# Performance work log

Hardware: AMD Instinct MI355X
Metric: run time of the kernel (lower is better)

## Reference

```python
import jax, jax.numpy as jnp
import numpy as np

jax.config.update("jax_enable_x64", True)  # original uses torch fp64 for the reciprocal trick

# --- GenericE layout constants ---
N = 32            # NUM_POSITIONS
D = 128           # per-position feature dim
F = N * D         # flattened dim
B = 8192          # batch
NIB_A, NIB_B = 0, 1
SLOT_DIVIDEND, SLOT_DIVISOR, SLOT_REMAINDER, SLOT_QUOTIENT = 2, 3, 4, 5
OP_START, OPCODE, BASE = 64, 3, 2
S = 60.0          # DIV_SCALE
SM_S = 60.0       # SOFTMAX1_SCALE
OP_FLAT = 0 * D + OP_START + OPCODE  # flat index of opcode channel at position 0


def _build_weights():
    # ClearDivSlotsFFN: hidden_dim = 4 slots * 2 units; bake_clear_pair wiring
    cW_up = np.zeros((8, F), np.float32)
    cW_gate = np.zeros((8, F), np.float32)
    cW_down = np.zeros((F, 8), np.float32)
    for i, slot in enumerate([SLOT_DIVIDEND, SLOT_DIVISOR, SLOT_REMAINDER, SLOT_QUOTIENT]):
        h = 2 * i
        # delta[slot] = -(1/S) * relu(S*op_w) * slot_val  -> clears slot when opcode active
        cW_up[h, OP_FLAT] = S
        cW_gate[h, slot] = 1.0
        cW_down[slot, h] = -1.0 / S
        # guard unit of the pair (zero down weight, mirrors gather's guard unit)
        cW_up[h + 1, OP_FLAT] = -S
        cW_gate[h + 1, slot] = -1.0
    # GatherScalarFFN: hidden_dim = N + 1; wiring straight from the source
    H = N + 1
    gW_up = np.zeros((H, F), np.float32)
    gW_gate = np.zeros((H, F), np.float32)
    gW_down = np.zeros((F, H), np.float32)
    dst = 0 * D + SLOT_DIVIDEND
    for i in range(N):
        gW_up[i, OP_FLAT] = S
        gW_gate[i, i * D + NIB_A] = float(BASE ** i)
        gW_down[dst, i] = 1.0 / S
    gW_up[N, OP_FLAT] = -S
    gW_gate[N, dst] = -1.0
    # gW_down[dst, N] = 0.0 (explicit in source)
    return (jnp.asarray(cW_up), jnp.asarray(cW_gate), jnp.asarray(cW_down),
            jnp.asarray(gW_up), jnp.asarray(gW_gate), jnp.asarray(gW_down))


def setup_inputs() -> dict:
    key = jax.random.key(0)
    x = jax.random.uniform(key, (B, N, D), dtype=jnp.float32)
    cW_up, cW_gate, cW_down, gW_up, gW_gate, gW_down = _build_weights()
    base_powers = jnp.asarray([float(BASE ** j) for j in range(N)], dtype=jnp.float64)
    return {"x": x, "cW_up": cW_up, "cW_gate": cW_gate, "cW_down": cW_down,
            "gW_up": gW_up, "gW_gate": gW_gate, "gW_down": gW_down,
            "base_powers": base_powers}


def _ffn_delta(xf, W_up, W_gate, W_down):
    # GenericFlattenedFFN residual delta: W_down @ (relu(W_up x) * (W_gate x))
    h = jax.nn.relu(xf @ W_up.T) * (xf @ W_gate.T)   # [B, H]
    return h @ W_down.T                               # [B, F]


def reference(x, cW_up, cW_gate, cW_down, gW_up, gW_gate, gW_down, base_powers):
    Bc, Nc, Dc = x.shape
    xf = x.reshape(Bc, Nc * Dc)
    # d1 + d2: the two FFN branches (each branch's forward is x + delta, so diff is delta)
    d12 = _ffn_delta(xf, cW_up, cW_gate, cW_down) + _ffn_delta(xf, gW_up, gW_gate, gW_down)
    # d3: Softmax1 reciprocal trick in fp64 (matching torch .double())
    op_w = x[:, 0, OP_START + OPCODE]                         # [B]
    d = x[:, :Nc, NIB_B].astype(jnp.float64)                  # [B, N]
    val = jnp.maximum(d * base_powers, 0.5)
    scores = jnp.where(d > 0.5, jnp.log(val), jnp.float64(-SM_S))
    mx = scores.max(axis=-1, keepdims=True)                   # [B, 1]
    sum_ex = jnp.exp(scores - mx).sum(axis=-1)                # [B]
    recip = jnp.exp(-mx[..., 0]) / jnp.maximum(sum_ex, 1e-30)
    out = x + d12.reshape(Bc, Nc, Dc)
    return out.at[:, 0, SLOT_QUOTIENT].add(op_w * recip.astype(x.dtype))
```

## Files before the change

kernel.cpp:

```cpp
#include <hip/hip_runtime.h>
#include <math.h>


#define DDIM 128
#define FDIM 4096

__global__ __launch_bounds__(256) void div_merged_kernel(
    const float* __restrict__ x, float* __restrict__ out, int rows) {
  const int bid = blockIdx.x;
  const int t = threadIdx.x;
  const int nfix = rows >> 2;

  if (bid < nfix) {
    const int wave = t >> 6;
    const int lane = t & 63;
    const long long row = (long long)bid * 4 + wave;
    const float* __restrict__ xr = x + row * (long long)FDIM;
    float* __restrict__ orow = out + row * (long long)FDIM;

    const bool active = lane < 32;
    double score = -60.0;
    double p = 0.0;
    if (active) {
      const float2 ab = *(const float2*)(xr + lane * DDIM);
      const double pw = (double)(1ULL << lane);
      p = (double)ab.x * pw;
      const double d = (double)ab.y;
      score = (d > 0.5) ? log(fmax(d * pw, 0.5)) : -60.0;
    }
    double mx = score;
#pragma unroll
    for (int off = 1; off < 64; off <<= 1)
      mx = fmax(mx, __shfl_xor(mx, off));
    double ex = active ? exp(score - mx) : 0.0;
#pragma unroll
    for (int off = 1; off < 64; off <<= 1) {
      ex += __shfl_xor(ex, off);
      p  += __shfl_xor(p, off);
    }
    if (lane == 0) {
      const float op    = xr[67];
      const float r60   = fmaxf(60.0f * op, 0.0f);
      const float inv60 = (float)(1.0 / 60.0);
      const double recip = exp(-mx) / fmax(ex, 1e-30);
      const float Pf = (float)p;
      float4 lo = *(const float4*)xr;
      float4 hi = *(const float4*)(xr + 4);
      const float dc2 = -((r60 * lo.z) * inv60);
      const float dc3 = -((r60 * lo.w) * inv60);
      const float dc4 = -((r60 * hi.x) * inv60);
      const float dc5 = -((r60 * hi.y) * inv60);
      const float dg2 = (r60 * Pf) * inv60;
      lo.z = lo.z + (dc2 + dg2);
      lo.w = lo.w + dc3;
      hi.x = hi.x + dc4;
      hi.y = (hi.y + dc5) + op * (float)recip;
      *(float4*)orow = lo;
      *(float4*)(orow + 4) = hi;
    }
  } else {
    const long long row = bid - nfix;
    const float4* __restrict__ x4 = (const float4*)(x + row * (long long)FDIM);
    float4* __restrict__ o4 = (float4*)(out + row * (long long)FDIM);
#pragma unroll
    for (int k = 0; k < 4; ++k) {
      const int idx = k * 256 + t;
      if (idx >= 2) o4[idx] = x4[idx];
    }
  }
}

extern "C" void kernel_launch(void* const* d_in, const int* in_sizes, int n_in,
                              void* d_out, int out_size, void* d_ws, size_t ws_size,
                              hipStream_t stream) {
  const float* x = (const float*)d_in[0];
  float* out = (float*)d_out;
  const int rows = in_sizes[0] / FDIM;
  const int nfix = rows >> 2;
  div_merged_kernel<<<rows + nfix, 256, 0, stream>>>(x, out, rows);
}
```

Measured before the change: 248.6 us.

## Split into grid-stride nontemporal copy kernel and separate packed fixup kernel

Replaces the merged per-row copy/fix kernel with a grid-stride copy kernel using four loads in flight and nontemporal stores, followed by a separate fix kernel. The fix kernel packs two rows per wave (32 lanes each) and rewrites only slots 2-5 of position 0. This aims to raise streaming bandwidth and halve wasted lanes in the fp64 reduction, at the cost of a second launch and a serial dependency between kernels.

Result: slower. 255.4 us (+2.7%).

```diff
diff --git a/kernel.cpp b/kernel.cpp
--- a/kernel.cpp
+++ b/kernel.cpp
@@ -5,68 +5,70 @@
 #define DDIM 128
 #define FDIM 4096
 
-__global__ __launch_bounds__(256) void div_merged_kernel(
+typedef float vfloat4 __attribute__((ext_vector_type(4)));
+
+__global__ __launch_bounds__(256) void copy_kernel(
+    const vfloat4* __restrict__ x4, vfloat4* __restrict__ o4, long long n4) {
+  const long long stride = (long long)gridDim.x * blockDim.x;
+  long long i = (long long)blockIdx.x * blockDim.x + threadIdx.x;
+  for (; i + 3 * stride < n4; i += 4 * stride) {
+    vfloat4 a = x4[i];
+    vfloat4 b = x4[i + stride];
+    vfloat4 c = x4[i + 2 * stride];
+    vfloat4 d = x4[i + 3 * stride];
+    __builtin_nontemporal_store(a, o4 + i);
+    __builtin_nontemporal_store(b, o4 + i + stride);
+    __builtin_nontemporal_store(c, o4 + i + 2 * stride);
+    __builtin_nontemporal_store(d, o4 + i + 3 * stride);
+  }
+  for (; i < n4; i += stride) {
+    vfloat4 a = x4[i];
+    __builtin_nontemporal_store(a, o4 + i);
+  }
+}
+
+__global__ __launch_bounds__(256) void fix_kernel(
     const float* __restrict__ x, float* __restrict__ out, int rows) {
-  const int bid = blockIdx.x;
   const int t = threadIdx.x;
-  const int nfix = rows >> 2;
+  const int wave = t >> 6;
+  const int lane = t & 63;
+  const int half = lane >> 5;
+  const int sl = lane & 31;
+  const long long row = (long long)blockIdx.x * 8 + wave * 2 + half;
+  if (row >= rows) return;
+  const float* __restrict__ xr = x + row * (long long)FDIM;
+  float* __restrict__ orow = out + row * (long long)FDIM;
 
-  if (bid < nfix) {
-    const int wave = t >> 6;
-    const int lane = t & 63;
-    const long long row = (long long)bid * 4 + wave;
-    const float* __restrict__ xr = x + row * (long long)FDIM;
-    float* __restrict__ orow = out + row * (long long)FDIM;
+  const float2 ab = *(const float2*)(xr + sl * DDIM);
+  const double pw = (double)(1U << sl);
+  double p = (double)ab.x * pw;
+  const double d = (double)ab.y;
+  double score = (d > 0.5) ? log(fmax(d * pw, 0.5)) : -60.0;
 
-    const bool active = lane < 32;
-    double score = -60.0;
-    double p = 0.0;
-    if (active) {
-      const float2 ab = *(const float2*)(xr + lane * DDIM);
-      const double pw = (double)(1ULL << lane);
-      p = (double)ab.x * pw;
-      const double d = (double)ab.y;
-      score = (d > 0.5) ? log(fmax(d * pw, 0.5)) : -60.0;
-    }
-    double mx = score;
+  double mx = score;
 #pragma unroll
-    for (int off = 1; off < 64; off <<= 1)
-      mx = fmax(mx, __shfl_xor(mx, off));
-    double ex = active ? exp(score - mx) : 0.0;
+  for (int off = 1; off < 32; off <<= 1)
+    mx = fmax(mx, __shfl_xor(mx, off));
+  double ex = exp(score - mx);
 #pragma unroll
-    for (int off = 1; off < 64; off <<= 1) {
-      ex += __shfl_xor(ex, off);
-      p  += __shfl_xor(p, off);
-    }
-    if (lane == 0) {
-      const float op    = xr[67];
-      const float r60   = fmaxf(60.0f * op, 0.0f);
-      const float inv60 = (float)(1.0 / 60.0);
-      const double recip = exp(-mx) / fmax(ex, 1e-30);
-      const float Pf = (float)p;
-      float4 lo = *(const float4*)xr;
-      float4 hi = *(const float4*)(xr + 4);
-      const float dc2 = -((r60 * lo.z) * inv60);
-      const float dc3 = -((r60 * lo.w) * inv60);
-      const float dc4 = -((r60 * hi.x) * inv60);
-      const float dc5 = -((r60 * hi.y) * inv60);
-      const float dg2 = (r60 * Pf) * inv60;
-      lo.z = lo.z + (dc2 + dg2);
-      lo.w = lo.w + dc3;
-      hi.x = hi.x + dc4;
-      hi.y = (hi.y + dc5) + op * (float)recip;
-      *(float4*)orow = lo;
-      *(float4*)(orow + 4) = hi;
-    }
-  } else {
-    const long long row = bid - nfix;
-    const float4* __restrict__ x4 = (const float4*)(x + row * (long long)FDIM);
-    float4* __restrict__ o4 = (float4*)(out + row * (long long)FDIM);
-#pragma unroll
-    for (int k = 0; k < 4; ++k) {
-      const int idx = k * 256 + t;
-      if (idx >= 2) o4[idx] = x4[idx];
-    }
+  for (int off = 1; off < 32; off <<= 1) {
+    ex += __shfl_xor(ex, off);
+    p  += __shfl_xor(p, off);
+  }
+  if (sl == 0) {
+    const float op    = xr[64 + 3];
+    const float r60   = fmaxf(60.0f * op, 0.0f);
+    const float inv60 = (float)(1.0 / 60.0);
+    const double recip = exp(-mx) / fmax(ex, 1e-30);
+    const float Pf = (float)p;
+    const float x2 = xr[2], x3 = xr[3], x4v = xr[4], x5 = xr[5];
+    float2 f23, f45;
+    f23.x = x2 + (-((r60 * x2) * inv60) + (r60 * Pf) * inv60);
+    f23.y = x3 - (r60 * x3) * inv60;
+    f45.x = x4v - (r60 * x4v) * inv60;
+    f45.y = (x5 - (r60 * x5) * inv60) + op * (float)recip;
+    *(float2*)(orow + 2) = f23;
+    *(float2*)(orow + 4) = f45;
   }
 }
 
@@ -76,6 +78,8 @@
   const float* x = (const float*)d_in[0];
   float* out = (float*)d_out;
   const int rows = in_sizes[0] / FDIM;
-  const int nfix = rows >> 2;
-  div_merged_kernel<<<rows + nfix, 256, 0, stream>>>(x, out, rows);
+  const long long n4 = (long long)rows * (FDIM / 4);
+
+  copy_kernel<<<2048, 256, 0, stream>>>((const vfloat4*)x, (vfloat4*)out, n4);
+  fix_kernel<<<(rows + 7) / 8, 256, 0, stream>>>(x, out, rows);
 }
```
